# Optimization experiments

Measured on AMD Instinct MI355X. Metric: run time of the kernel, lower is better.

The kernel has to match this reference:

```python
import jax, jax.numpy as jnp
import numpy as np

EPS = 1e-5

def setup_inputs() -> dict:
    key = jax.random.key(0)
    k1, k2, k3 = jax.random.split(key, 3)
    B, D, H = 8192, 1536, 16384
    x = jax.random.normal(k1, (B, D), dtype=jnp.float32)
    # torch Linear default init ~ U(-1/sqrt(fan_in), 1/sqrt(fan_in)); scaled normal is fine for a reference
    W_enc = jax.random.normal(k2, (H, D), dtype=jnp.float32) * (1.0 / np.sqrt(D))
    W_dec = jax.random.normal(k3, (D, H), dtype=jnp.float32) * (1.0 / np.sqrt(H))
    pre_bias = jnp.zeros((D,), dtype=jnp.float32)
    latent_bias = jnp.zeros((H,), dtype=jnp.float32)
    return {"x": x, "W_enc": W_enc, "W_dec": W_dec,
            "pre_bias": pre_bias, "latent_bias": latent_bias, "k": 64}


def reference(x, W_enc, W_dec, pre_bias, latent_bias, k):
    # ---- LN preprocess (torch .std uses Bessel correction, ddof=1) ----
    mu = jnp.mean(x, axis=-1, keepdims=True)          # [B,1]
    xc = x - mu
    std = jnp.std(xc, axis=-1, keepdims=True, ddof=1)  # [B,1]
    xn = xc / (std + EPS)

    # ---- encode: Linear(bias=False) on (xn - pre_bias), add latent_bias ----
    h = jnp.einsum('bd,hd->bh', xn - pre_bias, W_enc) + latent_bias  # [B,H]
    h = jax.nn.relu(h)

    # ---- topk sparsity: keep values >= k-th largest per row ----
    topk_vals = jax.lax.top_k(h, k)[0]                # [B,k]
    threshold = topk_vals[:, -1:]                     # [B,1]
    h_sparse = h * (h >= threshold)

    # ---- decode + denormalize ----
    recon = jnp.einsum('bh,dh->bd', h_sparse, W_dec) + pre_bias
    recon = recon * std + mu

    # ---- metrics (as arrays instead of .item()) ----
    sparsity_ratio = jnp.mean(jnp.mean((h_sparse == 0).astype(jnp.float32), axis=1))
    abs_h = jnp.abs(h_sparse)
    mean_activation = jnp.mean(abs_h)
    std_activation = jnp.std(abs_h, ddof=1)
    return recon, h_sparse, sparsity_ratio, mean_activation, std_activation
```

## Files before the change

### kernel.cpp

```cpp
#include <hip/hip_runtime.h>
#include <hip/hip_bf16.h>
#include <math.h>

static constexpr int Bn = 8192;
static constexpr int Hn = 16384;
static constexpr int Dn = 1536;
static constexpr int KTOP = 64;
static constexpr int KE = 1536;
static constexpr int WSTR = 2048;
static constexpr double EPSD = 1e-5;

static constexpr size_t MU_OFF  = 0;
static constexpr size_t STD_OFF = 32768;
static constexpr size_t CNT_OFF = 98304;
static constexpr size_t NNZ_OFF = 131072;
static constexpr size_t SUM_OFF = 131200;
static constexpr size_t MUD_OFF = 262144;
static constexpr size_t RID_OFF = 327680;
static constexpr size_t IDX_OFF = (size_t)1 << 20;
static constexpr size_t VAL_OFF = (size_t)6 << 20;
static constexpr size_t AP_OFF  = (size_t)16 << 20;
static constexpr size_t BP_OFF  = (size_t)48 << 20;
static constexpr size_t WT_OFF  = (size_t)104 << 20;
static constexpr size_t H16_OFF = (size_t)176 << 20;

typedef __attribute__((ext_vector_type(8))) short short8;
typedef __attribute__((ext_vector_type(4))) float f32x4;

static __device__ __forceinline__ unsigned short f2bf(float f) {
    __hip_bfloat16 b = __float2bfloat16(f);
    return *reinterpret_cast<unsigned short*>(&b);
}
static __device__ __forceinline__ float bf2f(unsigned short u) {
    return __uint_as_float(((unsigned)u) << 16);
}
static __device__ __forceinline__ void gload_lds16(const void* g, void* l) {
    __builtin_amdgcn_global_load_lds(
        (const __attribute__((address_space(1))) unsigned int*)g,
        (__attribute__((address_space(3))) unsigned int*)l, 16, 0, 0);
}

__global__ void k_zero(unsigned* nnz, double* sums) {
    if (threadIdx.x == 0) { *nnz = 0u; sums[0] = 0.0; sums[1] = 0.0; }
}

__global__ __launch_bounds__(256) void k_rowstats(const float* __restrict__ x,
                                                  const float* __restrict__ pre_bias,
                                                  double* __restrict__ muD,
                                                  double* __restrict__ rinvD,
                                                  float* __restrict__ muF,
                                                  float* __restrict__ stdF,
                                                  unsigned short* __restrict__ Ap) {
    const int row = blockIdx.x;
    const int tid = threadIdx.x;
    const float* xr = x + (size_t)row * Dn;
    float v[6];
#pragma unroll
    for (int i = 0; i < 6; ++i) v[i] = xr[tid + 256 * i];
    double s = 0.0;
#pragma unroll
    for (int i = 0; i < 6; ++i) s += (double)v[i];
    __shared__ double redD[4];
    __shared__ double smu, srin;
#pragma unroll
    for (int o = 32; o > 0; o >>= 1) s += __shfl_down(s, o);
    if ((tid & 63) == 0) redD[tid >> 6] = s;
    __syncthreads();
    if (tid == 0) smu = (redD[0] + redD[1] + redD[2] + redD[3]) / (double)Dn;
    __syncthreads();
    const double m = smu;
    double q = 0.0;
#pragma unroll
    for (int i = 0; i < 6; ++i) { double d = (double)v[i] - m; q += d * d; }
#pragma unroll
    for (int o = 32; o > 0; o >>= 1) q += __shfl_down(q, o);
    if ((tid & 63) == 0) redD[tid >> 6] = q;
    __syncthreads();
    if (tid == 0) {
        double var = (redD[0] + redD[1] + redD[2] + redD[3]) / (double)(Dn - 1);
        double sd = sqrt(var);
        muD[row] = m;
        srin = 1.0 / (sd + EPSD);
        rinvD[row] = srin;
        muF[row] = (float)m;
        stdF[row] = (float)sd;
    }
    __syncthreads();
    const double ri = srin;
    unsigned short* ar = Ap + (size_t)row * KE;
#pragma unroll
    for (int i = 0; i < 6; ++i) {
        const int d = tid + i * 256;
        double a = ((double)v[i] - m) * ri - (double)pre_bias[d];
        ar[d] = f2bf((float)a);
    }
}

__global__ __launch_bounds__(256) void k_splitW(const float* __restrict__ Wenc,
                                                unsigned short* __restrict__ Bp) {
    const int row = blockIdx.x;
    const int tid = threadIdx.x;
    const float2* wr = (const float2*)(Wenc + (size_t)row * Dn);
    ushort2* br = (ushort2*)(Bp + (size_t)row * KE);
#pragma unroll
    for (int i = 0; i < 3; ++i) {
        float2 w = wr[tid + i * 256];
        ushort2 o; o.x = f2bf(w.x); o.y = f2bf(w.y);
        br[tid + i * 256] = o;
    }
}

__global__ __launch_bounds__(256) void k_transpose(const float* __restrict__ Wdec,
                                                   unsigned short* __restrict__ WdecT) {
    __shared__ float tile[32][33];
    const int h0 = blockIdx.x * 32;
    const int d0 = blockIdx.y * 32;
    const int tx = threadIdx.x & 31;
    const int ty = threadIdx.x >> 5;
#pragma unroll
    for (int r = 0; r < 4; ++r) {
        int d = ty + r * 8;
        tile[d][tx] = Wdec[(size_t)(d0 + d) * Hn + h0 + tx];
    }
    __syncthreads();
#pragma unroll
    for (int r = 0; r < 4; ++r) {
        int h = ty + r * 8;
        WdecT[(size_t)(h0 + h) * WSTR + d0 + tx] = f2bf(tile[tx][h]);
    }
}

__global__ __launch_bounds__(512, 2) void k_gemm(const unsigned short* __restrict__ Ap,
                                                 const unsigned short* __restrict__ Bp,
                                                 const float* __restrict__ lat_bias,
                                                 unsigned short* __restrict__ hout16) {
    __shared__ unsigned short AsBuf[2][256 * 64];
    __shared__ unsigned short BsBuf[2][256 * 64];
    const int tid = threadIdx.x;
    const int lane = tid & 63;
    const int w = tid >> 6;
    const int wm = w >> 2;
    const int wn = w & 3;

    const int nwg = (Bn / 256) * (Hn / 256);
    int swz = (blockIdx.x % 8) * (nwg / 8) + blockIdx.x / 8;
    int st = swz >> 6;
    int wi = swz & 63;
    int stm = st >> 3, stn = st & 7;
    const int bm = stm * 8 + (wi >> 3);
    const int bn = stn * 8 + (wi & 7);

    const size_t arow0 = (size_t)(bm * 256) * KE;
    const size_t brow0 = (size_t)(bn * 256) * KE;

    #define STAGE_TILE(kt, buf)                                                   \
        {                                                                         \
            _Pragma("unroll")                                                     \
            for (int l = 0; l < 4; ++l) {                                         \
                const int idx = l * 512 + tid;                                    \
                const int row = idx >> 3, slot = idx & 7;                         \
                const int ssl = slot ^ (row & 7);                                 \
                gload_lds16(Ap + arow0 + (size_t)row * KE + (kt) * 64 + ssl * 8,  \
                            (char*)AsBuf[buf] + idx * 16);                        \
                gload_lds16(Bp + brow0 + (size_t)row * KE + (kt) * 64 + ssl * 8,  \
                            (char*)BsBuf[buf] + idx * 16);                        \
            }                                                                     \
        }

    f32x4 acc[8][4];
#pragma unroll
    for (int i = 0; i < 8; ++i)
#pragma unroll
        for (int j = 0; j < 4; ++j) acc[i][j] = (f32x4){0.f, 0.f, 0.f, 0.f};

    constexpr int NT = KE / 64;
    STAGE_TILE(0, 0);
    STAGE_TILE(1, 1);
    asm volatile("s_waitcnt vmcnt(8)" ::: "memory");
    __builtin_amdgcn_s_barrier();
    asm volatile("" ::: "memory");

    for (int t = 0; t < NT; ++t) {
        const int buf = t & 1;
        const unsigned short* Ab = AsBuf[buf];
        const unsigned short* Bb = BsBuf[buf];
        short8 bfr[4][2];
#pragma unroll
        for (int fj = 0; fj < 4; ++fj)
#pragma unroll
            for (int kk = 0; kk < 2; ++kk) {
                const int br = wn * 64 + fj * 16 + (lane & 15);
                const int slot = (kk * 4 + (lane >> 4)) ^ (br & 7);
                bfr[fj][kk] = *(const short8*)((const char*)Bb + br * 128 + slot * 16);
            }
#pragma unroll
        for (int qm = 0; qm < 2; ++qm) {
            short8 afr[4][2];
#pragma unroll
            for (int fi = 0; fi < 4; ++fi)
#pragma unroll
                for (int kk = 0; kk < 2; ++kk) {
                    const int ar = wm * 128 + qm * 64 + fi * 16 + (lane & 15);
                    const int slot = (kk * 4 + (lane >> 4)) ^ (ar & 7);
                    afr[fi][kk] = *(const short8*)((const char*)Ab + ar * 128 + slot * 16);
                }
#pragma unroll
            for (int kk = 0; kk < 2; ++kk)
#pragma unroll
                for (int fi = 0; fi < 4; ++fi)
#pragma unroll
                    for (int fj = 0; fj < 4; ++fj)
                        acc[qm * 4 + fi][fj] = __builtin_amdgcn_mfma_f32_16x16x32_bf16(
                            afr[fi][kk], bfr[fj][kk], acc[qm * 4 + fi][fj], 0, 0, 0);
        }
        __builtin_amdgcn_s_barrier();
        asm volatile("" ::: "memory");
        if (t + 2 < NT) {
            STAGE_TILE(t + 2, buf);
            asm volatile("s_waitcnt vmcnt(8)" ::: "memory");
        } else {
            asm volatile("s_waitcnt vmcnt(0)" ::: "memory");
        }
        __builtin_amdgcn_s_barrier();
        asm volatile("" ::: "memory");
    }
    #undef STAGE_TILE

    const int col = lane & 15;
#pragma unroll
    for (int fj = 0; fj < 4; ++fj) {
        const int gn = bn * 256 + wn * 64 + fj * 16 + col;
        const float bias = lat_bias[gn];
#pragma unroll
        for (int fi8 = 0; fi8 < 8; ++fi8) {
            const int gm0 = bm * 256 + wm * 128 + fi8 * 16 + (lane >> 4) * 4;
#pragma unroll
            for (int r = 0; r < 4; ++r) {
                float vv = acc[fi8][fj][r] + bias;
                hout16[(size_t)(gm0 + r) * Hn + gn] = f2bf(fmaxf(vv, 0.f));
            }
        }
    }
}

__global__ __launch_bounds__(256) void k_topsel(const unsigned short* __restrict__ h16,
                                                const float* __restrict__ x,
                                                const float* __restrict__ Wenc,
                                                const float* __restrict__ pre_bias,
                                                const float* __restrict__ lat_bias,
                                                const double* __restrict__ muD,
                                                const double* __restrict__ rinvD,
                                                unsigned* __restrict__ counts,
                                                int* __restrict__ idx_list,
                                                float* __restrict__ val_list) {
    const int row = blockIdx.x;
    const int tid = threadIdx.x;
    const int lane = tid & 63;
    const int wid = tid >> 6;
    const unsigned short* hr16 = h16 + (size_t)row * Hn;
    const unsigned* hu = (const unsigned*)hr16;
    unsigned u[32];
#pragma unroll
    for (int j = 0; j < 32; ++j) u[j] = hu[j * 256 + tid];

    __shared__ int wsum[4];
    __shared__ unsigned sbc;
    unsigned lo = 0, hi = 0xFFFFu;
    while (lo < hi) {
        const unsigned mid = (lo + hi + 1) >> 1;
        int c = 0;
#pragma unroll
        for (int j = 0; j < 32; ++j) {
            c += ((u[j] & 0xFFFFu) >= mid) ? 1 : 0;
            c += ((u[j] >> 16) >= mid) ? 1 : 0;
        }
#pragma unroll
        for (int o = 32; o > 0; o >>= 1) c += __shfl_down(c, o);
        if ((tid & 63) == 0) wsum[tid >> 6] = c;
        __syncthreads();
        if (tid == 0) sbc = (unsigned)(wsum[0] + wsum[1] + wsum[2] + wsum[3]);
        __syncthreads();
        if (sbc >= (unsigned)KTOP) lo = mid; else hi = mid - 1;
    }
    const float thr = bf2f((unsigned short)lo);
    const float DELTA = 0.02f;
    const float hi_t = thr + DELTA;
    const float lo_t = thr - DELTA;

    constexpr int MAXC = 128;
    __shared__ int s_g, s_c;
    __shared__ int cidx[MAXC];
    __shared__ double cvalD[MAXC];
    __shared__ float cref[MAXC];
    __shared__ unsigned char csel[MAXC];
    __shared__ unsigned long long kmask[256];
    __shared__ unsigned ccnt[256];
    __shared__ unsigned cinc[256];
    if (tid == 0) { s_g = 0; s_c = 0; }
    __syncthreads();
    int g_loc = 0;
#pragma unroll
    for (int j = 0; j < 32; ++j) {
        float v0 = bf2f((unsigned short)(u[j] & 0xFFFFu));
        float v1 = bf2f((unsigned short)(u[j] >> 16));
        const int i0 = 2 * (j * 256 + tid);
        if (v0 > hi_t) g_loc++;
        else if (v0 >= lo_t) {
            int p = atomicAdd(&s_c, 1);
            if (p < MAXC) cidx[p] = i0;
        }
        if (v1 > hi_t) g_loc++;
        else if (v1 >= lo_t) {
            int p = atomicAdd(&s_c, 1);
            if (p < MAXC) cidx[p] = i0 + 1;
        }
    }
    if (g_loc) atomicAdd(&s_g, g_loc);
    __syncthreads();
    const int ec = (s_c < MAXC) ? s_c : MAXC;

    {
        const double rmu = muD[row];
        const double rin = rinvD[row];
        const float* xr = x + (size_t)row * Dn;
        for (int e = wid; e < ec; e += 4) {
            const int feat = cidx[e];
            const float* wr = Wenc + (size_t)feat * Dn;
            double acc = 0.0;
            for (int d = lane; d < Dn; d += 64) {
                double xn = ((double)xr[d] - rmu) * rin - (double)pre_bias[d];
                acc = fma(xn, (double)wr[d], acc);
            }
#pragma unroll
            for (int o = 32; o > 0; o >>= 1) acc += __shfl_down(acc, o);
            if (lane == 0) {
                double hv = acc + (double)lat_bias[feat];
                cvalD[e] = hv;
                float hf = (float)hv;
                cref[e] = hf > 0.f ? hf : 0.f;
            }
        }
    }
    __syncthreads();
    if (tid == 0) {
        const int need = KTOP - s_g;
        for (int e = 0; e < ec; ++e) csel[e] = 0;
        for (int it = 0; it < need && it < ec; ++it) {
            int best = -1; double bv = -1e300; int bidx = 1 << 30;
            for (int e = 0; e < ec; ++e) {
                if (csel[e]) continue;
                if (cvalD[e] > bv || (cvalD[e] == bv && cidx[e] < bidx)) {
                    bv = cvalD[e]; best = e; bidx = cidx[e];
                }
            }
            if (best >= 0) csel[best] = 1;
        }
    }
    __syncthreads();

    for (int i = 0; i < 64; ++i) {
        const int c = wid * 64 + i;
        const int f = c * 64 + lane;
        float val = bf2f(hr16[f]);
        bool keep;
        if (val > hi_t) keep = true;
        else if (val >= lo_t) {
            keep = false;
            for (int e = 0; e < ec; ++e)
                if (cidx[e] == f) { keep = (csel[e] != 0); break; }
        } else keep = false;
        unsigned long long bm = __ballot(keep);
        if (lane == 0) { kmask[c] = bm; ccnt[c] = (unsigned)__popcll(bm); }
    }
    __syncthreads();
    cinc[tid] = ccnt[tid];
    __syncthreads();
#pragma unroll
    for (int o = 1; o < 256; o <<= 1) {
        unsigned t = cinc[tid] + ((tid >= o) ? cinc[tid - o] : 0u);
        __syncthreads();
        cinc[tid] = t;
        __syncthreads();
    }
    if (tid == 0) {
        unsigned tot = cinc[255];
        counts[row] = tot < 128u ? tot : 128u;
    }
    __syncthreads();
    for (int i = 0; i < 64; ++i) {
        const int c = wid * 64 + i;
        unsigned long long bm = kmask[c];
        if (!bm) continue;
        bool keep = (bm >> lane) & 1ull;
        if (keep) {
            unsigned pos = (cinc[c] - ccnt[c]) +
                           (unsigned)__popcll(bm & ((1ull << lane) - 1ull));
            if (pos < 128u) {
                const int f = c * 64 + lane;
                float sv = bf2f(hr16[f]);
                if (sv >= lo_t && sv <= hi_t) {
                    for (int e = 0; e < ec; ++e)
                        if (cidx[e] == f) { sv = cref[e]; break; }
                }
                idx_list[(size_t)row * 128 + pos] = f;
                val_list[(size_t)row * 128 + pos] = sv;
            }
        }
    }
}

__global__ __launch_bounds__(256) void k_hwdec(const unsigned* __restrict__ counts,
                                               const int* __restrict__ idx_list,
                                               const float* __restrict__ val_list,
                                               const unsigned short* __restrict__ WdecT,
                                               const float* __restrict__ pre_bias,
                                               const float* __restrict__ muF,
                                               const float* __restrict__ stdF,
                                               float* __restrict__ outh,
                                               float* __restrict__ outr,
                                               unsigned* __restrict__ nnz_acc,
                                               double* __restrict__ sums) {
    const int row = blockIdx.x;
    const int tid = threadIdx.x;
    const unsigned cnt = counts[row];
    __shared__ int sidx[128];
    __shared__ float sval[128];
    if (tid < (int)cnt) {
        sidx[tid] = idx_list[(size_t)row * 128 + tid];
        sval[tid] = val_list[(size_t)row * 128 + tid];
    }
    float* orow = outh + (size_t)row * Hn;
    float4* orow16 = (float4*)orow;
    const float4 z = {0.f, 0.f, 0.f, 0.f};
#pragma unroll
    for (int i = 0; i < 16; ++i) orow16[tid + i * 256] = z;
    __syncthreads();
    float val = 0.f;
    if (tid < (int)cnt) { orow[sidx[tid]] = sval[tid]; val = sval[tid]; }
    float s1 = val, s2 = val * val;
    __shared__ float r1[4], r2[4];
#pragma unroll
    for (int o = 32; o > 0; o >>= 1) {
        s1 += __shfl_down(s1, o);
        s2 += __shfl_down(s2, o);
    }
    if ((tid & 63) == 0) { r1[tid >> 6] = s1; r2[tid >> 6] = s2; }
    __syncthreads();
    if (tid == 0) {
        atomicAdd(sums + 0, (double)(r1[0] + r1[1] + r1[2] + r1[3]));
        atomicAdd(sums + 1, (double)(r2[0] + r2[1] + r2[2] + r2[3]));
        atomicAdd(nnz_acc, cnt);
    }
    if (tid >= 192) return;
    float a[8] = {0.f, 0.f, 0.f, 0.f, 0.f, 0.f, 0.f, 0.f};
    float b[8] = {0.f, 0.f, 0.f, 0.f, 0.f, 0.f, 0.f, 0.f};
    const size_t toff = (size_t)tid * 8;
    unsigned j = 0;
    for (; j + 2 <= cnt; j += 2) {
        short8 w0 = *(const short8*)(WdecT + (size_t)sidx[j] * WSTR + toff);
        short8 w1 = *(const short8*)(WdecT + (size_t)sidx[j + 1] * WSTR + toff);
        const float v0 = sval[j], v1 = sval[j + 1];
#pragma unroll
        for (int i = 0; i < 8; ++i) {
            a[i] = fmaf(v0, bf2f((unsigned short)w0[i]), a[i]);
            b[i] = fmaf(v1, bf2f((unsigned short)w1[i]), b[i]);
        }
    }
    if (j < cnt) {
        short8 w0 = *(const short8*)(WdecT + (size_t)sidx[j] * WSTR + toff);
        const float v0 = sval[j];
#pragma unroll
        for (int i = 0; i < 8; ++i)
            a[i] = fmaf(v0, bf2f((unsigned short)w0[i]), a[i]);
    }
    const float m_ = muF[row], s_ = stdF[row];
    const int d0 = tid * 8;
    float o[8];
#pragma unroll
    for (int i = 0; i < 8; ++i)
        o[i] = ((a[i] + b[i]) + pre_bias[d0 + i]) * s_ + m_;
    float* rrow = outr + (size_t)row * Dn + d0;
    *(float4*)(rrow)     = *(float4*)&o[0];
    *(float4*)(rrow + 4) = *(float4*)&o[4];
}

__global__ void k_final(const unsigned* __restrict__ nnz,
                        const double* __restrict__ sums,
                        float* __restrict__ out3) {
    if (threadIdx.x == 0) {
        const double N = (double)Bn * (double)Hn;
        const double nz = (double)(*nnz);
        const double sparsity = (N - nz) / N;
        const double mean = sums[0] / N;
        double var = (sums[1] - N * mean * mean) / (N - 1.0);
        if (var < 0.0) var = 0.0;
        out3[0] = (float)sparsity;
        out3[1] = (float)mean;
        out3[2] = (float)sqrt(var);
    }
}

extern "C" void kernel_launch(void* const* d_in, const int* in_sizes, int n_in,
                              void* d_out, int out_size, void* d_ws, size_t ws_size,
                              hipStream_t stream) {
    const float* x        = (const float*)d_in[0];
    const float* Wenc     = (const float*)d_in[1];
    const float* Wdec     = (const float*)d_in[2];
    const float* pre_bias = (const float*)d_in[3];
    const float* lat_bias = (const float*)d_in[4];

    char* ws = (char*)d_ws;
    float*          muF    = (float*)(ws + MU_OFF);
    float*          stdF   = (float*)(ws + STD_OFF);
    unsigned*       counts = (unsigned*)(ws + CNT_OFF);
    unsigned*       nnz    = (unsigned*)(ws + NNZ_OFF);
    double*         sums   = (double*)(ws + SUM_OFF);
    double*         muD    = (double*)(ws + MUD_OFF);
    double*         rinvD  = (double*)(ws + RID_OFF);
    int*            idxl   = (int*)(ws + IDX_OFF);
    float*          vall   = (float*)(ws + VAL_OFF);
    unsigned short* Ap     = (unsigned short*)(ws + AP_OFF);
    unsigned short* Bp     = (unsigned short*)(ws + BP_OFF);
    unsigned short* WdecT  = (unsigned short*)(ws + WT_OFF);
    unsigned short* h16    = (unsigned short*)(ws + H16_OFF);

    float* out       = (float*)d_out;
    float* out_recon = out;
    float* out_h     = out + (size_t)Bn * Dn;
    float* out_sc    = out + (size_t)Bn * Dn + (size_t)Bn * Hn;

    hipLaunchKernelGGL(k_zero, dim3(1), dim3(64), 0, stream, nnz, sums);
    hipLaunchKernelGGL(k_rowstats, dim3(Bn), dim3(256), 0, stream,
                       x, pre_bias, muD, rinvD, muF, stdF, Ap);
    hipLaunchKernelGGL(k_splitW, dim3(Hn), dim3(256), 0, stream, Wenc, Bp);
    hipLaunchKernelGGL(k_transpose, dim3(Hn / 32, Dn / 32), dim3(256), 0, stream, Wdec, WdecT);
    hipLaunchKernelGGL(k_gemm, dim3((Bn / 256) * (Hn / 256)), dim3(512), 0, stream,
                       Ap, Bp, lat_bias, h16);
    hipLaunchKernelGGL(k_topsel, dim3(Bn), dim3(256), 0, stream,
                       h16, x, Wenc, pre_bias, lat_bias, muD, rinvD,
                       counts, idxl, vall);
    hipLaunchKernelGGL(k_hwdec, dim3(Bn), dim3(256), 0, stream,
                       counts, idxl, vall, WdecT, pre_bias, muF, stdF,
                       out_h, out_recon, nnz, sums);
    hipLaunchKernelGGL(k_final, dim3(1), dim3(64), 0, stream, nnz, sums, out_sc);
}
```

Measured before the change: 1.393 ms.

## Stop threshold bisection early and finish on a compacted candidate set in LDS

The top-k threshold search over bf16 keys used to bisect all 16 bits by scanning 32 register-held values per thread on every step. It now stops once the number of keys inside the [lo,hi] bracket is at most 512. Those keys are compacted into shared memory and the remaining bisection runs over that small set. The register array is dropped, and each pass re-reads the row from global memory (L1/L2 resident) to cut register pressure and raise occupancy. The cost is extra global reads per scan and more barriers. It also depends on the bracket-count bookkeeping being correct, since the candidate cap can overflow.

Measured after the change: 1.863 ms. 1.34x slower.

```diff
diff --git a/kernel.cpp b/kernel.cpp
--- a/kernel.cpp
+++ b/kernel.cpp
@@ -259,20 +259,25 @@
     const int wid = tid >> 6;
     const unsigned short* hr16 = h16 + (size_t)row * Hn;
     const unsigned* hu = (const unsigned*)hr16;
-    unsigned u[32];
-#pragma unroll
-    for (int j = 0; j < 32; ++j) u[j] = hu[j * 256 + tid];
-
+
+    constexpr int MAXCOLL = 512;
     __shared__ int wsum[4];
     __shared__ unsigned sbc;
+    __shared__ unsigned short ckey[MAXCOLL];
+    __shared__ int s_ccount;
+
     unsigned lo = 0, hi = 0xFFFFu;
-    while (lo < hi) {
+    unsigned cl = 0x7FFFFFFFu;
+    unsigned ch = 0;
+    while (lo < hi && (cl - ch) > (unsigned)MAXCOLL) {
         const unsigned mid = (lo + hi + 1) >> 1;
         int c = 0;
 #pragma unroll
         for (int j = 0; j < 32; ++j) {
-            c += ((u[j] & 0xFFFFu) >= mid) ? 1 : 0;
-            c += ((u[j] >> 16) >= mid) ? 1 : 0;
+            const unsigned uu = hu[j * 256 + tid];
+            const unsigned k0 = uu & 0xFFFFu, k1 = uu >> 16;
+            c += (k0 >= mid) ? 1 : 0;
+            c += (k1 >= mid) ? 1 : 0;
         }
 #pragma unroll
         for (int o = 32; o > 0; o >>= 1) c += __shfl_down(c, o);
@@ -280,9 +285,52 @@
         __syncthreads();
         if (tid == 0) sbc = (unsigned)(wsum[0] + wsum[1] + wsum[2] + wsum[3]);
         __syncthreads();
-        if (sbc >= (unsigned)KTOP) lo = mid; else hi = mid - 1;
-    }
-    const float thr = bf2f((unsigned short)lo);
+        const unsigned cnt = sbc;
+        if (cnt >= (unsigned)KTOP) { lo = mid; cl = cnt; }
+        else                       { hi = mid - 1; ch = cnt; }
+        __syncthreads();
+    }
+
+    unsigned thr_key;
+    if (lo >= hi) {
+        thr_key = lo;
+    } else {
+        if (tid == 0) s_ccount = 0;
+        __syncthreads();
+#pragma unroll
+        for (int j = 0; j < 32; ++j) {
+            const unsigned uu = hu[j * 256 + tid];
+            const unsigned k0 = uu & 0xFFFFu, k1 = uu >> 16;
+            if (k0 && k0 >= lo && k0 <= hi) {
+                int p = atomicAdd(&s_ccount, 1);
+                if (p < MAXCOLL) ckey[p] = (unsigned short)k0;
+            }
+            if (k1 && k1 >= lo && k1 <= hi) {
+                int p = atomicAdd(&s_ccount, 1);
+                if (p < MAXCOLL) ckey[p] = (unsigned short)k1;
+            }
+        }
+        __syncthreads();
+        const int cc = (s_ccount < MAXCOLL) ? s_ccount : MAXCOLL;
+        const unsigned rem = (unsigned)KTOP - ch;
+        unsigned lo2 = lo, hi2 = hi;
+        while (lo2 < hi2) {
+            const unsigned mid = (lo2 + hi2 + 1) >> 1;
+            int c = 0;
+            if (tid < cc)       c += (ckey[tid] >= mid) ? 1 : 0;
+            if (tid + 256 < cc) c += (ckey[tid + 256] >= mid) ? 1 : 0;
+#pragma unroll
+            for (int o = 32; o > 0; o >>= 1) c += __shfl_down(c, o);
+            if ((tid & 63) == 0) wsum[tid >> 6] = c;
+            __syncthreads();
+            if (tid == 0) sbc = (unsigned)(wsum[0] + wsum[1] + wsum[2] + wsum[3]);
+            __syncthreads();
+            if (sbc >= rem) lo2 = mid; else hi2 = mid - 1;
+            __syncthreads();
+        }
+        thr_key = lo2;
+    }
+    const float thr = bf2f((unsigned short)thr_key);
     const float DELTA = 0.02f;
     const float hi_t = thr + DELTA;
     const float lo_t = thr - DELTA;
@@ -301,8 +349,9 @@
     int g_loc = 0;
 #pragma unroll
     for (int j = 0; j < 32; ++j) {
-        float v0 = bf2f((unsigned short)(u[j] & 0xFFFFu));
-        float v1 = bf2f((unsigned short)(u[j] >> 16));
+        const unsigned uu = hu[j * 256 + tid];
+        float v0 = bf2f((unsigned short)(uu & 0xFFFFu));
+        float v1 = bf2f((unsigned short)(uu >> 16));
         const int i0 = 2 * (j * 256 + tid);
         if (v0 > hi_t) g_loc++;
         else if (v0 >= lo_t) {
```
